# Kernel tuning notes

Hardware: AMD Instinct MI355X
Metric: run time of the kernel (lower is better)

Reference implementation:

```python
import jax, jax.numpy as jnp
import numpy as np

# Module constants (from __init__)
RADIUS = 1.0
VOXEL_SIZE = (0.16, 0.16)
PC_RANGE = (0.0, -25.6)
K = 4  # sample_points

M, N, C = 16384, 4096, 64
GRID = 320  # (51.2 - 0) / 0.16


def setup_inputs() -> dict:
    key = jax.random.key(0)
    k1, k2, k3, k4, k5 = jax.random.split(key, 5)
    pillar_feature = jax.random.normal(k1, (M, C), dtype=jnp.float32)
    # coors: (batch_id, z, y, x); single batch, z=0, y/x in BEV grid
    ys = jax.random.randint(k2, (M,), 0, GRID, dtype=jnp.int32)
    xs = jax.random.randint(k3, (M,), 0, GRID, dtype=jnp.int32)
    zeros = jnp.zeros((M,), dtype=jnp.int32)
    coors = jnp.stack([zeros, zeros, ys, xs], axis=1)  # [M, 4]
    seg_feats = jax.random.normal(k4, (N, C), dtype=jnp.float32)
    # seg points uniform in the BEV extent, z arbitrary (zeroed in forward)
    u = jax.random.uniform(k5, (N, 3), dtype=jnp.float32)
    seg_points = jnp.stack([
        u[:, 0] * 51.2 + 0.0,
        u[:, 1] * 51.2 - 25.6,
        u[:, 2] * 5.0 - 3.0,
    ], axis=1)  # [N, 3]
    return {"pillar_feature": pillar_feature, "coors": coors,
            "seg_feats": seg_feats, "seg_points": seg_points}


def _ball_query_idx(query_xy, pts_xy, radius, k_samples):
    """Replicates pointnet2/mmcv ball_query: for each query, the first
    k_samples in-radius point indices (scan order), slots padded with the
    first found index; all-zeros when no neighbor exists."""
    # [M, N] squared xy distance
    d2 = jnp.sum((query_xy[:, None, :] - pts_xy[None, :, :]) ** 2, axis=-1)
    within = d2 < radius * radius                       # [M, N]
    order = jnp.cumsum(within.astype(jnp.int32), axis=1)  # 1-based rank among in-radius pts
    slots = []
    for k in range(k_samples):  # small fixed K
        match = within & (order == k + 1)               # [M, N]
        has = jnp.any(match, axis=1)                    # [M]
        j = jnp.argmax(match, axis=1).astype(jnp.int32) # 0 when no match (CUDA zero-init)
        slots.append((has, j))
    first = slots[0][1]                                 # [M]
    idx = jnp.stack([jnp.where(h, j, first) for h, j in slots], axis=1)  # [M, K]
    return idx


def reference(pillar_feature, coors, seg_feats, seg_points):
    # get_pillar_center: x = (coors[:,3]+0.5)*vx + pc_x, y = (coors[:,2]+0.5)*vy + pc_y
    cf = coors.astype(jnp.float32)
    px = (cf[:, 3] + 0.5) * VOXEL_SIZE[0] + PC_RANGE[0]
    py = (cf[:, 2] + 0.5) * VOXEL_SIZE[1] + PC_RANGE[1]
    pillar_xy = jnp.stack([px, py], axis=1)             # [M, 2] (z zeroed in original)
    pts_xy = seg_points[:, :2]                          # z zeroed in original

    idx = _ball_query_idx(pillar_xy, pts_xy, RADIUS, K)  # [M, K] int32
    flag = (jnp.sum(idx, axis=1) > 0).astype(pillar_feature.dtype)  # [M]

    grouped = seg_feats[idx]                            # [M, K, C] gather
    pooled = jnp.max(grouped, axis=1)                   # max-pool over K samples
    return pillar_feature + pooled * flag[:, None]
```

## Files before the change

### kernel.cpp

```cpp
#include <hip/hip_runtime.h>

#define NPTS  4096
#define MQ    16384
#define CF    64
#define GRIDC 32
#define NCELLS (GRIDC * GRIDC)
#define CAP   20
#define INVCELL 0.625f
#define SENT  0x7fffffff
#define TPB   256
#define NBLK  512
#define QPB   (MQ / NBLK)

__global__ __launch_bounds__(TPB, 2) void k_all(
    const float* __restrict__ pillar,
    const int*   __restrict__ coors,
    const float* __restrict__ segf,
    const float* __restrict__ segp,
    float* __restrict__ out)
{
    __shared__ float2 sxy[NPTS];
    __shared__ int scnt[NCELLS];
    __shared__ unsigned short sbkt[NCELLS * CAP];

    const int tid = threadIdx.x;

    for (int c = tid; c < NCELLS; c += TPB) scnt[c] = 0;
    __syncthreads();

    for (int p = tid; p < NPTS; p += TPB) {
        const float px = segp[3 * p + 0];
        const float py = segp[3 * p + 1];
        sxy[p] = make_float2(px, py);
        int ix = (int)(px * INVCELL);
        int iy = (int)((py + 25.6f) * INVCELL);
        ix = min(max(ix, 0), GRIDC - 1);
        iy = min(max(iy, 0), GRIDC - 1);
        const int slot = atomicAdd(&scnt[iy * GRIDC + ix], 1);
        if (slot < CAP) sbkt[(iy * GRIDC + ix) * CAP + slot] = (unsigned short)p;
    }
    __syncthreads();

    const int wave = tid >> 6;
    const int lane = tid & 63;
    const int lc = lane / 20;
    const int sl = lane - lc * 20;

    for (int it = 0; it < QPB / 4; ++it) {
        const int q = blockIdx.x * QPB + wave * (QPB / 4) + it;
        const int cx = coors[4 * q + 3];
        const int cy = coors[4 * q + 2];
        const float qx = __fadd_rn(__fmul_rn(__fadd_rn((float)cx, 0.5f), 0.16f), 0.0f);
        const float qy = __fadd_rn(__fmul_rn(__fadd_rn((float)cy, 0.5f), 0.16f), -25.6f);
        const int icx = (int)(qx * INVCELL);
        const int icy = (int)((qy + 25.6f) * INVCELL);

        int c0 = SENT, c1 = SENT, c2 = SENT;
#pragma unroll
        for (int b = 0; b < 3; ++b) {
            int cand = SENT;
            if (lc < 3) {
                const int j = 3 * b + lc;
                const int iy2 = icy + j / 3 - 1;
                const int ix2 = icx + j % 3 - 1;
                if (ix2 >= 0 && ix2 < GRIDC && iy2 >= 0 && iy2 < GRIDC) {
                    const int cell = iy2 * GRIDC + ix2;
                    int cnt = scnt[cell];
                    cnt = cnt > CAP ? CAP : cnt;
                    if (sl < cnt) {
                        const int id = sbkt[cell * CAP + sl];
                        const float2 e = sxy[id];
                        const float dx = __fsub_rn(qx, e.x);
                        const float dy = __fsub_rn(qy, e.y);
                        const float d2 = __fadd_rn(__fmul_rn(dx, dx), __fmul_rn(dy, dy));
                        if (d2 < 1.0f) cand = id;
                    }
                }
            }
            if (cand < c2) {
                if (cand < c1) {
                    c2 = c1;
                    if (cand < c0) { c1 = c0; c0 = cand; } else { c1 = cand; }
                } else { c2 = cand; }
            }
        }

        int r0 = SENT, r1 = SENT, r2 = SENT, r3 = SENT;
#pragma unroll
        for (int r = 0; r < 4; ++r) {
            int v = c0;
            for (int off = 32; off; off >>= 1) v = min(v, __shfl_xor(v, off));
            if (v == SENT) break;
            if (r == 0) r0 = v; else if (r == 1) r1 = v;
            else if (r == 2) r2 = v; else r3 = v;
            if (c0 == v) { c0 = c1; c1 = c2; c2 = SENT; }
        }

        int i0, i1, i2, i3, flag;
        if (r0 == SENT) {
            i0 = i1 = i2 = i3 = 0; flag = 0;
        } else {
            i0 = r0;
            i1 = (r1 == SENT) ? r0 : r1;
            i2 = (r2 == SENT) ? r0 : r2;
            i3 = (r3 == SENT) ? r0 : r3;
            flag = (i0 + i1 + i2 + i3) > 0;
        }

        float m = 0.0f;
        if (flag) {
            const float a = segf[i0 * CF + lane];
            const float b2 = segf[i1 * CF + lane];
            const float c = segf[i2 * CF + lane];
            const float d = segf[i3 * CF + lane];
            m = fmaxf(fmaxf(a, b2), fmaxf(c, d));
        }
        out[q * CF + lane] = pillar[q * CF + lane] + m;
    }
}

extern "C" void kernel_launch(void* const* d_in, const int* in_sizes, int n_in,
                              void* d_out, int out_size, void* d_ws, size_t ws_size,
                              hipStream_t stream) {
    const float* pillar = (const float*)d_in[0];
    const int*   coors  = (const int*)d_in[1];
    const float* segf   = (const float*)d_in[2];
    const float* segp   = (const float*)d_in[3];
    float* out = (float*)d_out;

    k_all<<<NBLK, TPB, 0, stream>>>(pillar, coors, segf, segp, out);
}
```

Before: 83.92 us.

## Use 1024-thread blocks and bitonic top-4 wave merge for neighbor selection

Quadruples the threads per block so each wave handles fewer queries and the per-block LDS grid build is spread over more threads. This raises resident waves under the LDS-limited occupancy. Replaces the iterative four-round min-shuffle extraction with a butterfly merge of sorted top-4 lists across the wave, removing the serial rounds and the early-break branch. Larger blocks may raise register pressure, and the merge always pays for four shuffles per step.

```diff
diff --git a/kernel.cpp b/kernel.cpp
--- a/kernel.cpp
+++ b/kernel.cpp
@@ -8,11 +8,13 @@
 #define CAP   20
 #define INVCELL 0.625f
 #define SENT  0x7fffffff
-#define TPB   256
+#define TPB   1024
 #define NBLK  512
 #define QPB   (MQ / NBLK)
+#define WPB   (TPB / 64)
+#define QPW   (QPB / WPB)
 
-__global__ __launch_bounds__(TPB, 2) void k_all(
+__global__ __launch_bounds__(TPB) void k_all(
     const float* __restrict__ pillar,
     const int*   __restrict__ coors,
     const float* __restrict__ segf,
@@ -25,7 +27,7 @@
 
     const int tid = threadIdx.x;
 
-    for (int c = tid; c < NCELLS; c += TPB) scnt[c] = 0;
+    scnt[tid & (NCELLS - 1)] = 0;
     __syncthreads();
 
     for (int p = tid; p < NPTS; p += TPB) {
@@ -46,8 +48,8 @@
     const int lc = lane / 20;
     const int sl = lane - lc * 20;
 
-    for (int it = 0; it < QPB / 4; ++it) {
-        const int q = blockIdx.x * QPB + wave * (QPB / 4) + it;
+    for (int it = 0; it < QPW; ++it) {
+        const int q = blockIdx.x * QPB + wave * QPW + it;
         const int cx = coors[4 * q + 3];
         const int cy = coors[4 * q + 2];
         const float qx = __fadd_rn(__fmul_rn(__fadd_rn((float)cx, 0.5f), 0.16f), 0.0f);
@@ -85,25 +87,31 @@
             }
         }
 
-        int r0 = SENT, r1 = SENT, r2 = SENT, r3 = SENT;
+        int v0 = c0, v1 = c1, v2 = c2, v3 = SENT;
 #pragma unroll
-        for (int r = 0; r < 4; ++r) {
-            int v = c0;
-            for (int off = 32; off; off >>= 1) v = min(v, __shfl_xor(v, off));
-            if (v == SENT) break;
-            if (r == 0) r0 = v; else if (r == 1) r1 = v;
-            else if (r == 2) r2 = v; else r3 = v;
-            if (c0 == v) { c0 = c1; c1 = c2; c2 = SENT; }
+        for (int off = 1; off < 64; off <<= 1) {
+            const int w0 = __shfl_xor(v0, off);
+            const int w1 = __shfl_xor(v1, off);
+            const int w2 = __shfl_xor(v2, off);
+            const int w3 = __shfl_xor(v3, off);
+            const int t0 = min(v0, w3);
+            const int t1 = min(v1, w2);
+            const int t2 = min(v2, w1);
+            const int t3 = min(v3, w0);
+            const int a0 = min(t0, t2), a2 = max(t0, t2);
+            const int a1 = min(t1, t3), a3 = max(t1, t3);
+            v0 = min(a0, a1); v1 = max(a0, a1);
+            v2 = min(a2, a3); v3 = max(a2, a3);
         }
 
         int i0, i1, i2, i3, flag;
-        if (r0 == SENT) {
+        if (v0 == SENT) {
             i0 = i1 = i2 = i3 = 0; flag = 0;
         } else {
-            i0 = r0;
-            i1 = (r1 == SENT) ? r0 : r1;
-            i2 = (r2 == SENT) ? r0 : r2;
-            i3 = (r3 == SENT) ? r0 : r3;
+            i0 = v0;
+            i1 = (v1 == SENT) ? v0 : v1;
+            i2 = (v2 == SENT) ? v0 : v2;
+            i3 = (v3 == SENT) ? v0 : v3;
             flag = (i0 + i1 + i2 + i3) > 0;
         }
 
```

Measured after the change: 70.44 us. 16.1% less time.
